# Kernel tuning notes

Measured on AMD Instinct MI355X. Metric: run time of the kernel, lower is better.

## Reference

```python
import jax, jax.numpy as jnp
import numpy as np

C = 256
G = 16
EPS = 1e-5


def conv1x1(x, w):
    # x: [N,C,H,W], w: [Cout,Cin]
    return jnp.einsum('nchw,oc->nohw', x, w)


def group_norm(x, gamma, beta, groups=G, eps=EPS):
    n, c, h, w = x.shape
    xg = x.reshape(n, groups, c // groups, h, w)
    mu = xg.mean(axis=(2, 3, 4), keepdims=True)
    var = ((xg - mu) ** 2).mean(axis=(2, 3, 4), keepdims=True)
    xn = ((xg - mu) * jax.lax.rsqrt(var + eps)).reshape(n, c, h, w)
    return xn * gamma[:, None, None] + beta[:, None, None]


def silu(x):
    return x * jax.nn.sigmoid(x)


def scan(x, axis, reverse=False):
    if reverse:
        return jnp.flip(jnp.cumsum(jnp.flip(x, axis), axis=axis), axis)
    return jnp.cumsum(x, axis=axis)


def depthwise3x3(x, w_dw):
    # w_dw: [C,1,3,3], groups=C
    return jax.lax.conv_general_dilated(
        x, w_dw, window_strides=(1, 1), padding=((1, 1), (1, 1)),
        dimension_numbers=('NCHW', 'OIHW', 'NCHW'), feature_group_count=x.shape[1])


def setup_inputs() -> dict:
    key = jax.random.key(0)
    ks = jax.random.split(key, 5)
    N, H, W = 8, 80, 80
    s1 = 1.0 / np.sqrt(C)
    return {
        'x': jax.random.normal(ks[0], (N, C, H, W), jnp.float32),
        'w_pre': jax.random.normal(ks[1], (C, C), jnp.float32) * s1,
        'g1': jnp.ones((C,), jnp.float32),
        'b1': jnp.zeros((C,), jnp.float32),
        'w_gate': jax.random.normal(ks[2], (C, C), jnp.float32) * s1,
        'b_gate': jnp.zeros((C,), jnp.float32),
        'w_dw': jax.random.normal(ks[3], (C, 1, 3, 3), jnp.float32) * (1.0 / 3.0),
        'w_pw': jax.random.normal(ks[4], (C, C), jnp.float32) * s1,
        'g2': jnp.ones((C,), jnp.float32),
        'b2': jnp.zeros((C,), jnp.float32),
    }


def reference(x, w_pre, g1, b1, w_gate, b_gate, w_dw, w_pw, g2, b2):
    # pre: 1x1 conv -> GroupNorm -> SiLU
    h = silu(group_norm(conv1x1(x, w_pre), g1, b1))
    # 4-directional cumulative scans
    lr = scan(h, 3, False)
    rl = scan(h, 3, True)
    tb = scan(h, 2, False)
    bt = scan(h, 2, True)
    fused = (lr + rl + tb + bt) * 0.25
    # sigmoid gate from pre features
    gate = jax.nn.sigmoid(conv1x1(h, w_gate) + b_gate[:, None, None])
    gated = fused * gate
    # mix: depthwise 3x3 -> 1x1 -> GroupNorm -> SiLU
    y = depthwise3x3(gated, w_dw)
    y = conv1x1(y, w_pw)
    return silu(group_norm(y, g2, b2))
```

## Files before the change

### kernel.cpp

```cpp
#include <hip/hip_runtime.h>
#include <stdint.h>

#define CC 256
#define HH 80
#define WW 80
#define PP 6400
#define GG 16
#define GNCNT (16*6400)
#define SAPAD 272

using frag_ab = __attribute__((ext_vector_type(8))) short;
using frag_cd = __attribute__((ext_vector_type(4))) float;
typedef unsigned short u16;

__device__ __forceinline__ float b2f(u16 u) {
    union { float f; uint32_t i; } v; v.i = ((uint32_t)u) << 16; return v.f;
}
__device__ __forceinline__ u16 f2b(float f) {
    uint32_t x = __float_as_uint(f);
    return (u16)((x + 0x7fffu + ((x >> 16) & 1u)) >> 16);
}
__device__ __forceinline__ float sigf(float x) { return 1.f / (1.f + __expf(-x)); }

__global__ __launch_bounds__(256) void cvt_kernel(const float* __restrict__ src,
                                                  u16* __restrict__ dst, int n4) {
    int i = blockIdx.x * 256 + threadIdx.x;
    if (i < n4) {
        float4 v = ((const float4*)src)[i];
        ushort4 o;
        o.x = f2b(v.x); o.y = f2b(v.y); o.z = f2b(v.z); o.w = f2b(v.w);
        ((ushort4*)dst)[i] = o;
    }
}

template<int MODE>
__global__ __launch_bounds__(256, 3) void gemm_kernel(
    const u16* __restrict__ A,
    const u16* __restrict__ Wb,
    u16* __restrict__ Out,
    float* __restrict__ pstats,
    const float* __restrict__ Srow,
    const float* __restrict__ Scol,
    const float* __restrict__ bgate,
    const float* __restrict__ Xf)
{
    __shared__ __align__(16) u16 sA[64 * SAPAD];

    const int t    = threadIdx.x;
    const int lane = t & 63;
    const int wave = t >> 6;
    const int m    = lane & 15;
    const int q    = lane >> 4;
    const int mt   = blockIdx.x;
    const int m0   = mt * 64;
    const int n    = mt / 100;
    const int o0w  = wave * 64;

    if (MODE == 0) {
        const int cl = t >> 2, pq = t & 3;
        const int p0 = m0 - n * PP;
        #pragma unroll
        for (int cb = 0; cb < 4; cb++) {
            const int c = cb * 64 + cl;
            const float* row = Xf + ((size_t)(n * CC + c)) * PP + p0 + pq * 16;
            #pragma unroll
            for (int u = 0; u < 4; u++) {
                float4 v = ((const float4*)(row + u * 4))[0];
                const int pp = pq * 16 + u * 4;
                sA[(pp + 0) * SAPAD + c] = f2b(v.x);
                sA[(pp + 1) * SAPAD + c] = f2b(v.y);
                sA[(pp + 2) * SAPAD + c] = f2b(v.z);
                sA[(pp + 3) * SAPAD + c] = f2b(v.w);
            }
        }
    } else {
        const int row = t >> 2, qt = t & 3;
        const u16* g = A + (size_t)(m0 + row) * CC + qt * 64;
        u16* d = sA + row * SAPAD + qt * 64;
        #pragma unroll
        for (int i = 0; i < 8; i++)
            *(frag_ab*)(d + i * 8) = *(const frag_ab*)(g + i * 8);
    }
    __syncthreads();

    frag_cd acc[4][4];
    #pragma unroll
    for (int ms = 0; ms < 4; ms++)
        #pragma unroll
        for (int j = 0; j < 4; j++)
            #pragma unroll
            for (int k = 0; k < 4; k++) acc[ms][j][k] = 0.f;

    const u16* wl = Wb + (size_t)(o0w + m) * CC + q * 8;

    #pragma unroll
    for (int jh = 0; jh < 2; jh++) {
        frag_ab wf[2][8];
        #pragma unroll
        for (int jj = 0; jj < 2; jj++)
            #pragma unroll
            for (int kc = 0; kc < 8; kc++)
                wf[jj][kc] = *(const frag_ab*)(wl + (size_t)((jh * 2 + jj) * 16) * CC + kc * 32);
        #pragma unroll
        for (int jj = 0; jj < 2; jj++)
            #pragma unroll
            for (int kc = 0; kc < 8; kc++)
                asm volatile("" : "+v"(wf[jj][kc]));

        #pragma unroll
        for (int ms = 0; ms < 4; ms++) {
            #pragma unroll
            for (int kc = 0; kc < 8; kc++) {
                frag_ab af = *(const frag_ab*)(sA + (ms * 16 + m) * SAPAD + kc * 32 + q * 8);
                #pragma unroll
                for (int jj = 0; jj < 2; jj++)
                    acc[ms][jh * 2 + jj] = __builtin_amdgcn_mfma_f32_16x16x32_bf16(
                        af, wf[jj][kc], acc[ms][jh * 2 + jj], 0, 0, 0);
            }
        }
    }

    ushort4 hv[4][4];
    if (MODE == 1) {
        const int rr0 = lane >> 4;
        const int cH  = o0w + (lane & 15) * 4;
        #pragma unroll
        for (int ms = 0; ms < 4; ms++)
            #pragma unroll
            for (int u = 0; u < 4; u++)
                hv[ms][u] = *(const ushort4*)(sA + (size_t)(ms * 16 + u * 4 + rr0) * SAPAD + cH);
    }
    __syncthreads();

    if (MODE == 0 || MODE == 2) {
        #pragma unroll
        for (int j = 0; j < 4; j++) {
            float s = 0.f, sq = 0.f;
            #pragma unroll
            for (int ms = 0; ms < 4; ms++)
                #pragma unroll
                for (int r = 0; r < 4; r++) {
                    float v = acc[ms][j][r];
                    s += v; sq += v * v;
                }
            #pragma unroll
            for (int off = 32; off > 0; off >>= 1) {
                s  += __shfl_down(s, off);
                sq += __shfl_down(sq, off);
            }
            if (lane == 0) {
                float* p = pstats + (size_t)mt * 32;
                p[wave * 4 + j]      = s;
                p[16 + wave * 4 + j] = sq;
            }
        }
        u16* myT = sA + wave * 1152;
        #pragma unroll
        for (int ms = 0; ms < 4; ms++) {
            #pragma unroll
            for (int j = 0; j < 4; j++)
                #pragma unroll
                for (int r = 0; r < 4; r++)
                    myT[(q * 4 + r) * 72 + j * 16 + m] = f2b(acc[ms][j][r]);
            #pragma unroll
            for (int u = 0; u < 2; u++) {
                const int rr = u * 8 + (lane >> 3);
                frag_ab v = *(const frag_ab*)(myT + rr * 72 + (lane & 7) * 8);
                *(frag_ab*)(Out + (size_t)(m0 + ms * 16 + rr) * CC + o0w + (lane & 7) * 8) = v;
            }
        }
    } else {
        float* myG = (float*)sA + wave * 1152;
        float bg[4];
        #pragma unroll
        for (int j = 0; j < 4; j++) bg[j] = bgate[o0w + j * 16 + m];
        #pragma unroll
        for (int ms = 0; ms < 4; ms++) {
            #pragma unroll
            for (int j = 0; j < 4; j++)
                #pragma unroll
                for (int r = 0; r < 4; r++)
                    myG[(q * 4 + r) * 72 + j * 16 + m] = sigf(acc[ms][j][r] + bg[j]);
            #pragma unroll
            for (int u = 0; u < 4; u++) {
                const int rr  = u * 4 + (lane >> 4);
                const int col = (lane & 15) * 4;
                float4 g4 = *(const float4*)(myG + rr * 72 + col);
                const int row = m0 + ms * 16 + rr;
                const int pl  = row - n * PP;
                const int pr  = pl / WW;
                const int pc  = pl - pr * WW;
                const int o   = o0w + col;
                ushort4 hq = hv[ms][u];
                float4  sr = *(const float4*)(Srow + (size_t)(n * HH + pr) * CC + o);
                float4  sc = *(const float4*)(Scol + (size_t)(n * HH + pc) * CC + o);
                ushort4 ov;
                ov.x = f2b(0.25f * (sr.x + sc.x + 2.f * b2f(hq.x)) * g4.x);
                ov.y = f2b(0.25f * (sr.y + sc.y + 2.f * b2f(hq.y)) * g4.y);
                ov.z = f2b(0.25f * (sr.z + sc.z + 2.f * b2f(hq.z)) * g4.z);
                ov.w = f2b(0.25f * (sr.w + sc.w + 2.f * b2f(hq.w)) * g4.w);
                *(ushort4*)(Out + (size_t)row * CC + o) = ov;
            }
        }
    }
}

__global__ __launch_bounds__(256) void gn1_kernel(
    const u16* __restrict__ c1, u16* __restrict__ hb,
    float* __restrict__ Srow,
    const float* __restrict__ pscr,
    const float* __restrict__ g1, const float* __restrict__ b1)
{
    __shared__ float sred[8 * 256];
    __shared__ float sstat[32];
    const int i = blockIdx.x, n = blockIdx.y;
    const int t = threadIdx.x;
    if (t < 32) {
        const int kind = t >> 4, g = t & 15;
        const float* p = pscr + (size_t)(n * 100) * 32 + kind * 16 + g;
        float s = 0.f;
        #pragma unroll 4
        for (int ii = 0; ii < 100; ii++) s += p[ii * 32];
        sstat[t] = s;
    }
    __syncthreads();

    const int jg = t >> 5, cc = t & 31;
    const int c8 = cc * 8;
    const int g  = cc >> 1;
    const float su   = sstat[g];
    const float sq   = sstat[16 + g];
    const float mean = su * (1.f / GNCNT);
    const float var  = sq * (1.f / GNCNT) - mean * mean;
    const float inv  = rsqrtf(var + 1e-5f);
    float a[8], b[8];
    #pragma unroll
    for (int k = 0; k < 8; k++) {
        a[k] = inv * g1[c8 + k];
        b[k] = b1[c8 + k] - mean * a[k];
    }
    float srow8[8];
    #pragma unroll
    for (int k = 0; k < 8; k++) srow8[k] = 0.f;

    const size_t base = (size_t)(n * PP + i * WW) * CC;
    for (int s = 0; s < 10; s++) {
        const int j = jg + s * 8;
        const u16* src = c1 + base + (size_t)j * CC + c8;
        u16*       dst = hb + base + (size_t)j * CC + c8;
        frag_ab v = *(const frag_ab*)src;
        frag_ab o;
        #pragma unroll
        for (int k = 0; k < 8; k++) {
            float xn = b2f((u16)v[k]) * a[k] + b[k];
            float hs = xn * sigf(xn);
            o[k] = (short)f2b(hs);
            srow8[k] += hs;
        }
        *(frag_ab*)dst = o;
    }
    #pragma unroll
    for (int k = 0; k < 8; k++) sred[jg * 256 + c8 + k] = srow8[k];
    __syncthreads();
    {
        const int c = t;
        float s = 0.f;
        #pragma unroll
        for (int k = 0; k < 8; k++) s += sred[k * 256 + c];
        Srow[(size_t)(n * HH + i) * CC + c] = s;
    }
}

__global__ __launch_bounds__(256) void scol_kernel(
    const u16* __restrict__ hb, float* __restrict__ Scol)
{
    const int jg = blockIdx.x, iq = blockIdx.y, n = blockIdx.z;
    const int t = threadIdx.x;
    const int js = t >> 5, cc = t & 31;
    const int j = jg * 8 + js, c8 = cc * 8;
    float acc8[8];
    #pragma unroll
    for (int k = 0; k < 8; k++) acc8[k] = 0.f;
    for (int s = 0; s < 20; s++) {
        const int i = iq * 20 + s;
        frag_ab v = *(const frag_ab*)(hb + (size_t)(n * PP + i * WW + j) * CC + c8);
        #pragma unroll
        for (int k = 0; k < 8; k++) acc8[k] += b2f((u16)v[k]);
    }
    float* dst = Scol + (size_t)(n * HH + j) * CC + c8;
    #pragma unroll
    for (int k = 0; k < 8; k++) atomicAdd(&dst[k], acc8[k]);
}

__global__ __launch_bounds__(256) void dw_kernel(
    const u16* __restrict__ gin, u16* __restrict__ dout,
    const float* __restrict__ wdw)
{
    __shared__ float sw[1152];
    const int i = blockIdx.x, chalf = blockIdx.y, n = blockIdx.z;
    const int t = threadIdx.x;
    for (int u = t; u < 1152; u += 256) sw[u] = wdw[chalf * 1152 + u];
    __syncthreads();

    const int jg = t >> 5, cc = t & 31;
    const int gc = chalf * 128 + cc * 4;
    float wl[4][9];
    #pragma unroll
    for (int cl = 0; cl < 4; cl++)
        #pragma unroll
        for (int k = 0; k < 9; k++) wl[cl][k] = sw[(cc * 4 + cl) * 9 + k];

    const size_t nbase = (size_t)n * PP * CC;
    for (int s = 0; s < 10; s++) {
        const int j = jg + s * 8;
        float acc4[4] = {0.f, 0.f, 0.f, 0.f};
        #pragma unroll
        for (int di = -1; di <= 1; di++) {
            const int ii = i + di;
            if (ii < 0 || ii >= HH) continue;
            #pragma unroll
            for (int dj = -1; dj <= 1; dj++) {
                const int jj = j + dj;
                if (jj < 0 || jj >= WW) continue;
                ushort4 v = *(const ushort4*)(gin + nbase + (size_t)(ii * WW + jj) * CC + gc);
                const int k = (di + 1) * 3 + (dj + 1);
                acc4[0] += wl[0][k] * b2f(v.x);
                acc4[1] += wl[1][k] * b2f(v.y);
                acc4[2] += wl[2][k] * b2f(v.z);
                acc4[3] += wl[3][k] * b2f(v.w);
            }
        }
        ushort4 o;
        o.x = f2b(acc4[0]); o.y = f2b(acc4[1]); o.z = f2b(acc4[2]); o.w = f2b(acc4[3]);
        *(ushort4*)(dout + nbase + (size_t)(i * WW + j) * CC + gc) = o;
    }
}

__global__ __launch_bounds__(256) void gn2T_kernel(
    const u16* __restrict__ Y, float* __restrict__ out,
    const float* __restrict__ pscr,
    const float* __restrict__ g2, const float* __restrict__ b2v)
{
    __shared__ u16 sT[64 * 72];
    __shared__ float sstat[32];
    const int p0 = blockIdx.x * 64, c0 = blockIdx.y * 64, n = blockIdx.z;
    const int t = threadIdx.x;
    if (t < 32) {
        const int kind = t >> 4, g = t & 15;
        const float* p = pscr + (size_t)(n * 100) * 32 + kind * 16 + g;
        float s = 0.f;
        #pragma unroll 4
        for (int ii = 0; ii < 100; ii++) s += p[ii * 32];
        sstat[t] = s;
    }
    {
        const int pl = t >> 2, cq = t & 3;
        const u16* row = Y + (size_t)(n * PP + p0 + pl) * CC + c0 + cq * 16;
        *(frag_ab*)(sT + pl * 72 + cq * 16)     = *(const frag_ab*)(row);
        *(frag_ab*)(sT + pl * 72 + cq * 16 + 8) = *(const frag_ab*)(row + 8);
    }
    __syncthreads();
    {
        const int cl = t >> 2, pq = t & 3;
        const int c = c0 + cl, g = c >> 4;
        const float su   = sstat[g];
        const float sq   = sstat[16 + g];
        const float mean = su * (1.f / GNCNT);
        const float var  = sq * (1.f / GNCNT) - mean * mean;
        const float inv  = rsqrtf(var + 1e-5f);
        const float a    = inv * g2[c];
        const float b    = b2v[c] - mean * a;
        float* orow = out + (size_t)(n * CC + c) * PP + p0 + pq * 16;
        #pragma unroll
        for (int u4 = 0; u4 < 4; u4++) {
            float4 o;
            float* op = (float*)&o;
            #pragma unroll
            for (int e = 0; e < 4; e++) {
                const int pp = pq * 16 + u4 * 4 + e;
                float xn = b2f(sT[pp * 72 + cl]) * a + b;
                op[e] = xn * sigf(xn);
            }
            ((float4*)(orow + u4 * 4))[0] = o;
        }
    }
}

extern "C" void kernel_launch(void* const* d_in, const int* in_sizes, int n_in,
                              void* d_out, int out_size, void* d_ws, size_t ws_size,
                              hipStream_t stream)
{
    const float* x      = (const float*)d_in[0];
    const float* w_pre  = (const float*)d_in[1];
    const float* g1     = (const float*)d_in[2];
    const float* b1     = (const float*)d_in[3];
    const float* w_gate = (const float*)d_in[4];
    const float* b_gate = (const float*)d_in[5];
    const float* w_dw   = (const float*)d_in[6];
    const float* w_pw   = (const float*)d_in[7];
    const float* g2     = (const float*)d_in[8];
    const float* b2     = (const float*)d_in[9];
    float* out = (float*)d_out;

    char* ws = (char*)d_ws;
    u16*   wb0   = (u16*)(ws);
    u16*   wb1   = (u16*)(ws + 131072);
    u16*   wb2   = (u16*)(ws + 262144);
    u16*   bufA  = (u16*)(ws + 26607616);
    u16*   bufB  = (u16*)(ws + 52822016);
    float* Srow  = (float*)(ws + 79036416);
    float* Scol  = (float*)(ws + 79691776);
    float* pscr0 = (float*)(ws + 80347136);
    float* pscr1 = (float*)(ws + 80449536);

    hipMemsetAsync(Scol, 0, 655360, stream);

    cvt_kernel<<<64, 256, 0, stream>>>(w_pre,  wb0, 16384);
    cvt_kernel<<<64, 256, 0, stream>>>(w_gate, wb1, 16384);
    cvt_kernel<<<64, 256, 0, stream>>>(w_pw,   wb2, 16384);

    gemm_kernel<0><<<800, 256, 0, stream>>>(nullptr, wb0, bufA, pscr0,
                                            nullptr, nullptr, nullptr, x);
    gn1_kernel<<<dim3(80, 8), 256, 0, stream>>>(bufA, bufB, Srow, pscr0, g1, b1);
    scol_kernel<<<dim3(10, 4, 8), 256, 0, stream>>>(bufB, Scol);
    gemm_kernel<1><<<800, 256, 0, stream>>>(bufB, wb1, bufA, nullptr,
                                            Srow, Scol, b_gate, nullptr);
    dw_kernel<<<dim3(80, 2, 8), 256, 0, stream>>>(bufA, bufB, w_dw);
    gemm_kernel<2><<<800, 256, 0, stream>>>(bufB, wb2, bufA, pscr1,
                                            nullptr, nullptr, nullptr, nullptr);
    gn2T_kernel<<<dim3(100, 4, 8), 256, 0, stream>>>(bufA, out, pscr1, g2, b2);
}
```

Baseline: 305.6 us.

## Process two tiles per GEMM block with register prefetch; drop atomics and memset

GEMM modes 1 and 2 now launch 400 blocks, and each block handles two 64-row tiles. The second tile's A data is prefetched into registers while the first tile computes, then written to LDS. The scol kernel writes per-quarter partial column sums instead of using atomicAdd, which removes the memset; the gate GEMM epilogue sums the four partials. The three weight conversions are merged into one launch, and some barriers become explicit waitcnt+s_barrier. The cost is more register pressure (launch bounds occupancy drops to 2 for these modes) and four times more Scol reads in the epilogue.

Measured after the change: 324.4 us. 6.1% more time.

```diff
diff --git a/kernel.cpp b/kernel.cpp
--- a/kernel.cpp
+++ b/kernel.cpp
@@ -22,66 +22,38 @@
 }
 __device__ __forceinline__ float sigf(float x) { return 1.f / (1.f + __expf(-x)); }
 
-__global__ __launch_bounds__(256) void cvt_kernel(const float* __restrict__ src,
-                                                  u16* __restrict__ dst, int n4) {
-    int i = blockIdx.x * 256 + threadIdx.x;
-    if (i < n4) {
-        float4 v = ((const float4*)src)[i];
-        ushort4 o;
-        o.x = f2b(v.x); o.y = f2b(v.y); o.z = f2b(v.z); o.w = f2b(v.w);
-        ((ushort4*)dst)[i] = o;
-    }
-}
+__device__ __forceinline__ void bar_lgkm() {
+    asm volatile("s_waitcnt lgkmcnt(0)\n\ts_barrier" ::: "memory");
+}
+
+__global__ __launch_bounds__(256) void cvt3_kernel(
+    const float* __restrict__ s0, const float* __restrict__ s1,
+    const float* __restrict__ s2,
+    u16* __restrict__ d0, u16* __restrict__ d1, u16* __restrict__ d2)
+{
+    const int blk = blockIdx.x >> 6;
+    const int i = (blockIdx.x & 63) * 256 + threadIdx.x;
+    const float* s = (blk == 0) ? s0 : (blk == 1) ? s1 : s2;
+    u16*         d = (blk == 0) ? d0 : (blk == 1) ? d1 : d2;
+    float4 v = ((const float4*)s)[i];
+    ushort4 o;
+    o.x = f2b(v.x); o.y = f2b(v.y); o.z = f2b(v.z); o.w = f2b(v.w);
+    ((ushort4*)d)[i] = o;
+}
+
 
 template<int MODE>
-__global__ __launch_bounds__(256, 3) void gemm_kernel(
-    const u16* __restrict__ A,
+__device__ __forceinline__ void tile_body(
+    u16* sA, int mt,
     const u16* __restrict__ Wb,
-    u16* __restrict__ Out,
-    float* __restrict__ pstats,
-    const float* __restrict__ Srow,
-    const float* __restrict__ Scol,
+    u16* __restrict__ Out, float* __restrict__ pstats,
+    const float* __restrict__ Srow, const float* __restrict__ Scolp,
     const float* __restrict__ bgate,
-    const float* __restrict__ Xf)
-{
-    __shared__ __align__(16) u16 sA[64 * SAPAD];
-
-    const int t    = threadIdx.x;
-    const int lane = t & 63;
-    const int wave = t >> 6;
-    const int m    = lane & 15;
-    const int q    = lane >> 4;
-    const int mt   = blockIdx.x;
-    const int m0   = mt * 64;
-    const int n    = mt / 100;
-    const int o0w  = wave * 64;
-
-    if (MODE == 0) {
-        const int cl = t >> 2, pq = t & 3;
-        const int p0 = m0 - n * PP;
-        #pragma unroll
-        for (int cb = 0; cb < 4; cb++) {
-            const int c = cb * 64 + cl;
-            const float* row = Xf + ((size_t)(n * CC + c)) * PP + p0 + pq * 16;
-            #pragma unroll
-            for (int u = 0; u < 4; u++) {
-                float4 v = ((const float4*)(row + u * 4))[0];
-                const int pp = pq * 16 + u * 4;
-                sA[(pp + 0) * SAPAD + c] = f2b(v.x);
-                sA[(pp + 1) * SAPAD + c] = f2b(v.y);
-                sA[(pp + 2) * SAPAD + c] = f2b(v.z);
-                sA[(pp + 3) * SAPAD + c] = f2b(v.w);
-            }
-        }
-    } else {
-        const int row = t >> 2, qt = t & 3;
-        const u16* g = A + (size_t)(m0 + row) * CC + qt * 64;
-        u16* d = sA + row * SAPAD + qt * 64;
-        #pragma unroll
-        for (int i = 0; i < 8; i++)
-            *(frag_ab*)(d + i * 8) = *(const frag_ab*)(g + i * 8);
-    }
-    __syncthreads();
+    int lane, int wave, int m, int q)
+{
+    const int m0  = mt * 64;
+    const int n   = mt / 100;
+    const int o0w = wave * 64;
 
     frag_cd acc[4][4];
     #pragma unroll
@@ -130,7 +102,7 @@
             for (int u = 0; u < 4; u++)
                 hv[ms][u] = *(const ushort4*)(sA + (size_t)(ms * 16 + u * 4 + rr0) * SAPAD + cH);
     }
-    __syncthreads();
+    bar_lgkm();
 
     if (MODE == 0 || MODE == 2) {
         #pragma unroll
@@ -193,7 +165,12 @@
                 const int o   = o0w + col;
                 ushort4 hq = hv[ms][u];
                 float4  sr = *(const float4*)(Srow + (size_t)(n * HH + pr) * CC + o);
-                float4  sc = *(const float4*)(Scol + (size_t)(n * HH + pc) * CC + o);
+                float4 sc; sc.x = sc.y = sc.z = sc.w = 0.f;
+                #pragma unroll
+                for (int iq = 0; iq < 4; iq++) {
+                    float4 v = *(const float4*)(Scolp + ((size_t)((iq * 8 + n) * HH + pc)) * CC + o);
+                    sc.x += v.x; sc.y += v.y; sc.z += v.z; sc.w += v.w;
+                }
                 ushort4 ov;
                 ov.x = f2b(0.25f * (sr.x + sc.x + 2.f * b2f(hq.x)) * g4.x);
                 ov.y = f2b(0.25f * (sr.y + sc.y + 2.f * b2f(hq.y)) * g4.y);
@@ -203,6 +180,87 @@
             }
         }
     }
+}
+
+template<int MODE>
+__global__ __launch_bounds__(256, (MODE == 0 ? 3 : 2)) void gemm_kernel(
+    const u16* __restrict__ A,
+    const u16* __restrict__ Wb,
+    u16* __restrict__ Out,
+    float* __restrict__ pstats,
+    const float* __restrict__ Srow,
+    const float* __restrict__ Scolp,
+    const float* __restrict__ bgate,
+    const float* __restrict__ Xf)
+{
+    __shared__ __align__(16) u16 sA[64 * SAPAD];
+
+    const int t    = threadIdx.x;
+    const int lane = t & 63;
+    const int wave = t >> 6;
+    const int m    = lane & 15;
+    const int q    = lane >> 4;
+
+    if (MODE == 0) {
+        const int mt = blockIdx.x;
+        const int n  = mt / 100;
+        const int cl = t >> 2, pq = t & 3;
+        const int p0 = mt * 64 - n * PP;
+        #pragma unroll
+        for (int cb = 0; cb < 4; cb++) {
+            const int c = cb * 64 + cl;
+            const float* row = Xf + ((size_t)(n * CC + c)) * PP + p0 + pq * 16;
+            #pragma unroll
+            for (int u = 0; u < 4; u++) {
+                float4 v = ((const float4*)(row + u * 4))[0];
+                const int pp = pq * 16 + u * 4;
+                sA[(pp + 0) * SAPAD + c] = f2b(v.x);
+                sA[(pp + 1) * SAPAD + c] = f2b(v.y);
+                sA[(pp + 2) * SAPAD + c] = f2b(v.z);
+                sA[(pp + 3) * SAPAD + c] = f2b(v.w);
+            }
+        }
+        __syncthreads();
+        tile_body<MODE>(sA, mt, Wb, Out, pstats, Srow, Scolp, bgate, lane, wave, m, q);
+        return;
+    }
+
+    const int mt0 = blockIdx.x;
+    const int mt1 = blockIdx.x + 400;
+    const int row = t >> 2, qt = t & 3;
+
+    {
+        const u16* g = A + (size_t)(mt0 * 64 + row) * CC + qt * 64;
+        u16* d = sA + row * SAPAD + qt * 64;
+        #pragma unroll
+        for (int i = 0; i < 8; i++)
+            *(frag_ab*)(d + i * 8) = *(const frag_ab*)(g + i * 8);
+    }
+    __syncthreads();
+
+    frag_ab P[8];
+    {
+        const u16* g = A + (size_t)(mt1 * 64 + row) * CC + qt * 64;
+        #pragma unroll
+        for (int i = 0; i < 8; i++)
+            P[i] = *(const frag_ab*)(g + i * 8);
+        #pragma unroll
+        for (int i = 0; i < 8; i++)
+            asm volatile("" : "+v"(P[i]));
+    }
+
+    tile_body<MODE>(sA, mt0, Wb, Out, pstats, Srow, Scolp, bgate, lane, wave, m, q);
+
+    bar_lgkm();
+    {
+        u16* d = sA + row * SAPAD + qt * 64;
+        #pragma unroll
+        for (int i = 0; i < 8; i++)
+            *(frag_ab*)(d + i * 8) = P[i];
+    }
+    bar_lgkm();
+
+    tile_body<MODE>(sA, mt1, Wb, Out, pstats, Srow, Scolp, bgate, lane, wave, m, q);
 }
 
 __global__ __launch_bounds__(256) void gn1_kernel(
@@ -272,7 +330,7 @@
 }
 
 __global__ __launch_bounds__(256) void scol_kernel(
-    const u16* __restrict__ hb, float* __restrict__ Scol)
+    const u16* __restrict__ hb, float* __restrict__ Scolp)
 {
     const int jg = blockIdx.x, iq = blockIdx.y, n = blockIdx.z;
     const int t = threadIdx.x;
@@ -287,9 +345,9 @@
         #pragma unroll
         for (int k = 0; k < 8; k++) acc8[k] += b2f((u16)v[k]);
     }
-    float* dst = Scol + (size_t)(n * HH + j) * CC + c8;
-    #pragma unroll
-    for (int k = 0; k < 8; k++) atomicAdd(&dst[k], acc8[k]);
+    float* dst = Scolp + ((size_t)((iq * 8 + n) * HH + j)) * CC + c8;
+    *(float4*)(dst)     = make_float4(acc8[0], acc8[1], acc8[2], acc8[3]);
+    *(float4*)(dst + 4) = make_float4(acc8[4], acc8[5], acc8[6], acc8[7]);
 }
 
 __global__ __launch_bounds__(256) void dw_kernel(
@@ -406,27 +464,23 @@
     u16*   wb0   = (u16*)(ws);
     u16*   wb1   = (u16*)(ws + 131072);
     u16*   wb2   = (u16*)(ws + 262144);
+    float* Scolp = (float*)(ws + 393216);
     u16*   bufA  = (u16*)(ws + 26607616);
     u16*   bufB  = (u16*)(ws + 52822016);
     float* Srow  = (float*)(ws + 79036416);
-    float* Scol  = (float*)(ws + 79691776);
     float* pscr0 = (float*)(ws + 80347136);
     float* pscr1 = (float*)(ws + 80449536);
 
-    hipMemsetAsync(Scol, 0, 655360, stream);
-
-    cvt_kernel<<<64, 256, 0, stream>>>(w_pre,  wb0, 16384);
-    cvt_kernel<<<64, 256, 0, stream>>>(w_gate, wb1, 16384);
-    cvt_kernel<<<64, 256, 0, stream>>>(w_pw,   wb2, 16384);
+    cvt3_kernel<<<192, 256, 0, stream>>>(w_pre, w_gate, w_pw, wb0, wb1, wb2);
 
     gemm_kernel<0><<<800, 256, 0, stream>>>(nullptr, wb0, bufA, pscr0,
                                             nullptr, nullptr, nullptr, x);
     gn1_kernel<<<dim3(80, 8), 256, 0, stream>>>(bufA, bufB, Srow, pscr0, g1, b1);
-    scol_kernel<<<dim3(10, 4, 8), 256, 0, stream>>>(bufB, Scol);
-    gemm_kernel<1><<<800, 256, 0, stream>>>(bufB, wb1, bufA, nullptr,
-                                            Srow, Scol, b_gate, nullptr);
+    scol_kernel<<<dim3(10, 4, 8), 256, 0, stream>>>(bufB, Scolp);
+    gemm_kernel<1><<<400, 256, 0, stream>>>(bufB, wb1, bufA, nullptr,
+                                            Srow, Scolp, b_gate, nullptr);
     dw_kernel<<<dim3(80, 2, 8), 256, 0, stream>>>(bufA, bufB, w_dw);
-    gemm_kernel<2><<<800, 256, 0, stream>>>(bufB, wb2, bufA, pscr1,
+    gemm_kernel<2><<<400, 256, 0, stream>>>(bufB, wb2, bufA, pscr1,
                                             nullptr, nullptr, nullptr, nullptr);
     gn2T_kernel<<<dim3(100, 4, 8), 256, 0, stream>>>(bufA, out, pscr1, g2, b2);
 }
```

## Fuse depthwise 3x3 conv into pointwise GEMM prologue and merge weight conversions

Applied to the files above, without the earlier changes.

The separate depthwise 3x3 kernel is removed. Each pointwise GEMM block now computes the depthwise conv for its 64 pixel rows straight into shared-memory A tiles, which avoids writing and re-reading the full intermediate bf16 tensor. The three weight-conversion launches are merged into one kernel. The cost is extra shared memory for the transposed weights, an extra barrier, and redundant halo loads inside the GEMM prologue, which may lower occupancy.

Result: slower. 352.9 us (+15.5%).

```diff
diff --git a/kernel.cpp b/kernel.cpp
--- a/kernel.cpp
+++ b/kernel.cpp
@@ -22,15 +22,19 @@
 }
 __device__ __forceinline__ float sigf(float x) { return 1.f / (1.f + __expf(-x)); }
 
-__global__ __launch_bounds__(256) void cvt_kernel(const float* __restrict__ src,
-                                                  u16* __restrict__ dst, int n4) {
-    int i = blockIdx.x * 256 + threadIdx.x;
-    if (i < n4) {
-        float4 v = ((const float4*)src)[i];
-        ushort4 o;
-        o.x = f2b(v.x); o.y = f2b(v.y); o.z = f2b(v.z); o.w = f2b(v.w);
-        ((ushort4*)dst)[i] = o;
-    }
+__global__ __launch_bounds__(256) void cvt3_kernel(
+    const float* __restrict__ s0, const float* __restrict__ s1,
+    const float* __restrict__ s2,
+    u16* __restrict__ d0, u16* __restrict__ d1, u16* __restrict__ d2)
+{
+    const int blk = blockIdx.x >> 6;
+    const int i = (blockIdx.x & 63) * 256 + threadIdx.x;
+    const float* s = (blk == 0) ? s0 : (blk == 1) ? s1 : s2;
+    u16*         d = (blk == 0) ? d0 : (blk == 1) ? d1 : d2;
+    float4 v = ((const float4*)s)[i];
+    ushort4 o;
+    o.x = f2b(v.x); o.y = f2b(v.y); o.z = f2b(v.z); o.w = f2b(v.w);
+    ((ushort4*)d)[i] = o;
 }
 
 template<int MODE>
@@ -42,9 +46,10 @@
     const float* __restrict__ Srow,
     const float* __restrict__ Scol,
     const float* __restrict__ bgate,
-    const float* __restrict__ Xf)
+    const float* __restrict__ Xfw)
 {
     __shared__ __align__(16) u16 sA[64 * SAPAD];
+    __shared__ float sw[(MODE == 2) ? 2304 : 1];
 
     const int t    = threadIdx.x;
     const int lane = t & 63;
@@ -62,7 +67,7 @@
         #pragma unroll
         for (int cb = 0; cb < 4; cb++) {
             const int c = cb * 64 + cl;
-            const float* row = Xf + ((size_t)(n * CC + c)) * PP + p0 + pq * 16;
+            const float* row = Xfw + ((size_t)(n * CC + c)) * PP + p0 + pq * 16;
             #pragma unroll
             for (int u = 0; u < 4; u++) {
                 float4 v = ((const float4*)(row + u * 4))[0];
@@ -72,6 +77,41 @@
                 sA[(pp + 2) * SAPAD + c] = f2b(v.z);
                 sA[(pp + 3) * SAPAD + c] = f2b(v.w);
             }
+        }
+    } else if (MODE == 2) {
+        for (int u = t; u < 2304; u += 256) {
+            const int c = u / 9, k = u - c * 9;
+            sw[k * 256 + c] = Xfw[u];
+        }
+        __syncthreads();
+        const int cc4 = (lane) * 4;
+        const int r0  = wave;
+        float4 wl[9];
+        #pragma unroll
+        for (int k = 0; k < 9; k++)
+            wl[k] = *(const float4*)(sw + k * 256 + cc4);
+        for (int s = 0; s < 16; s++) {
+            const int r  = r0 + s * 4;
+            const int p  = m0 + r - n * PP;
+            const int pr = p / WW, pc = p - pr * WW;
+            float a0 = 0.f, a1 = 0.f, a2 = 0.f, a3 = 0.f;
+            #pragma unroll
+            for (int di = -1; di <= 1; di++) {
+                const int ii = pr + di;
+                if (ii < 0 || ii >= HH) continue;
+                #pragma unroll
+                for (int dj = -1; dj <= 1; dj++) {
+                    const int jj = pc + dj;
+                    if (jj < 0 || jj >= WW) continue;
+                    ushort4 v = *(const ushort4*)(A + (size_t)(n * PP + ii * WW + jj) * CC + cc4);
+                    const float4 w = wl[(di + 1) * 3 + (dj + 1)];
+                    a0 += w.x * b2f(v.x); a1 += w.y * b2f(v.y);
+                    a2 += w.z * b2f(v.z); a3 += w.w * b2f(v.w);
+                }
+            }
+            ushort4 o;
+            o.x = f2b(a0); o.y = f2b(a1); o.z = f2b(a2); o.w = f2b(a3);
+            *(ushort4*)(sA + r * SAPAD + cc4) = o;
         }
     } else {
         const int row = t >> 2, qt = t & 3;
@@ -292,50 +332,6 @@
     for (int k = 0; k < 8; k++) atomicAdd(&dst[k], acc8[k]);
 }
 
-__global__ __launch_bounds__(256) void dw_kernel(
-    const u16* __restrict__ gin, u16* __restrict__ dout,
-    const float* __restrict__ wdw)
-{
-    __shared__ float sw[1152];
-    const int i = blockIdx.x, chalf = blockIdx.y, n = blockIdx.z;
-    const int t = threadIdx.x;
-    for (int u = t; u < 1152; u += 256) sw[u] = wdw[chalf * 1152 + u];
-    __syncthreads();
-
-    const int jg = t >> 5, cc = t & 31;
-    const int gc = chalf * 128 + cc * 4;
-    float wl[4][9];
-    #pragma unroll
-    for (int cl = 0; cl < 4; cl++)
-        #pragma unroll
-        for (int k = 0; k < 9; k++) wl[cl][k] = sw[(cc * 4 + cl) * 9 + k];
-
-    const size_t nbase = (size_t)n * PP * CC;
-    for (int s = 0; s < 10; s++) {
-        const int j = jg + s * 8;
-        float acc4[4] = {0.f, 0.f, 0.f, 0.f};
-        #pragma unroll
-        for (int di = -1; di <= 1; di++) {
-            const int ii = i + di;
-            if (ii < 0 || ii >= HH) continue;
-            #pragma unroll
-            for (int dj = -1; dj <= 1; dj++) {
-                const int jj = j + dj;
-                if (jj < 0 || jj >= WW) continue;
-                ushort4 v = *(const ushort4*)(gin + nbase + (size_t)(ii * WW + jj) * CC + gc);
-                const int k = (di + 1) * 3 + (dj + 1);
-                acc4[0] += wl[0][k] * b2f(v.x);
-                acc4[1] += wl[1][k] * b2f(v.y);
-                acc4[2] += wl[2][k] * b2f(v.z);
-                acc4[3] += wl[3][k] * b2f(v.w);
-            }
-        }
-        ushort4 o;
-        o.x = f2b(acc4[0]); o.y = f2b(acc4[1]); o.z = f2b(acc4[2]); o.w = f2b(acc4[3]);
-        *(ushort4*)(dout + nbase + (size_t)(i * WW + j) * CC + gc) = o;
-    }
-}
-
 __global__ __launch_bounds__(256) void gn2T_kernel(
     const u16* __restrict__ Y, float* __restrict__ out,
     const float* __restrict__ pscr,
@@ -415,9 +411,7 @@
 
     hipMemsetAsync(Scol, 0, 655360, stream);
 
-    cvt_kernel<<<64, 256, 0, stream>>>(w_pre,  wb0, 16384);
-    cvt_kernel<<<64, 256, 0, stream>>>(w_gate, wb1, 16384);
-    cvt_kernel<<<64, 256, 0, stream>>>(w_pw,   wb2, 16384);
+    cvt3_kernel<<<192, 256, 0, stream>>>(w_pre, w_gate, w_pw, wb0, wb1, wb2);
 
     gemm_kernel<0><<<800, 256, 0, stream>>>(nullptr, wb0, bufA, pscr0,
                                             nullptr, nullptr, nullptr, x);
@@ -425,8 +419,7 @@
     scol_kernel<<<dim3(10, 4, 8), 256, 0, stream>>>(bufB, Scol);
     gemm_kernel<1><<<800, 256, 0, stream>>>(bufB, wb1, bufA, nullptr,
                                             Srow, Scol, b_gate, nullptr);
-    dw_kernel<<<dim3(80, 2, 8), 256, 0, stream>>>(bufA, bufB, w_dw);
-    gemm_kernel<2><<<800, 256, 0, stream>>>(bufB, wb2, bufA, pscr1,
-                                            nullptr, nullptr, nullptr, nullptr);
-    gn2T_kernel<<<dim3(100, 4, 8), 256, 0, stream>>>(bufA, out, pscr1, g2, b2);
-}
+    gemm_kernel<2><<<800, 256, 0, stream>>>(bufA, wb2, bufB, pscr1,
+                                            nullptr, nullptr, nullptr, w_dw);
+    gn2T_kernel<<<dim3(100, 4, 8), 256, 0, stream>>>(bufB, out, pscr1, g2, b2);
+}
```

## Recompute GroupNorm1+SiLU in consumers instead of materializing activations

Applied to the files above, without the earlier changes.

The normalized and activated tensor h is no longer written to global memory. The row-sum, column-sum and gate-GEMM kernels each read the raw conv output and recompute GroupNorm and SiLU from the partial statistics; the gate GEMM does this while staging its A tile into shared memory. The aim is to remove one full bf16 activation write and the pass that produced it. In exchange each consumer recomputes the sigmoid, and the group statistics are reduced redundantly in every block. The three weight-conversion launches are also merged into one kernel.

After: 318.1 us. 1.04x slower.

```diff
diff --git a/kernel.cpp b/kernel.cpp
--- a/kernel.cpp
+++ b/kernel.cpp
@@ -22,15 +22,19 @@
 }
 __device__ __forceinline__ float sigf(float x) { return 1.f / (1.f + __expf(-x)); }
 
-__global__ __launch_bounds__(256) void cvt_kernel(const float* __restrict__ src,
-                                                  u16* __restrict__ dst, int n4) {
-    int i = blockIdx.x * 256 + threadIdx.x;
-    if (i < n4) {
-        float4 v = ((const float4*)src)[i];
-        ushort4 o;
-        o.x = f2b(v.x); o.y = f2b(v.y); o.z = f2b(v.z); o.w = f2b(v.w);
-        ((ushort4*)dst)[i] = o;
-    }
+__global__ __launch_bounds__(256) void cvt3_kernel(
+    const float* __restrict__ s0, const float* __restrict__ s1,
+    const float* __restrict__ s2,
+    u16* __restrict__ d0, u16* __restrict__ d1, u16* __restrict__ d2)
+{
+    const int blk = blockIdx.x >> 6;
+    const int i = (blockIdx.x & 63) * 256 + threadIdx.x;
+    const float* s = (blk == 0) ? s0 : (blk == 1) ? s1 : s2;
+    u16*         d = (blk == 0) ? d0 : (blk == 1) ? d1 : d2;
+    float4 v = ((const float4*)s)[i];
+    ushort4 o;
+    o.x = f2b(v.x); o.y = f2b(v.y); o.z = f2b(v.z); o.w = f2b(v.w);
+    ((ushort4*)d)[i] = o;
 }
 
 template<int MODE>
@@ -42,9 +46,13 @@
     const float* __restrict__ Srow,
     const float* __restrict__ Scol,
     const float* __restrict__ bgate,
-    const float* __restrict__ Xf)
+    const float* __restrict__ Xf,
+    const float* __restrict__ g1v,
+    const float* __restrict__ b1v)
 {
     __shared__ __align__(16) u16 sA[64 * SAPAD];
+    __shared__ float sstat[32];
+    __shared__ float sAB[512];
 
     const int t    = threadIdx.x;
     const int lane = t & 63;
@@ -72,6 +80,41 @@
                 sA[(pp + 2) * SAPAD + c] = f2b(v.z);
                 sA[(pp + 3) * SAPAD + c] = f2b(v.w);
             }
+        }
+    } else if (MODE == 1) {
+        if (t < 32) {
+            const int kind = t >> 4, g = t & 15;
+            const float* p = pstats + (size_t)(n * 100) * 32 + kind * 16 + g;
+            float s = 0.f;
+            #pragma unroll 4
+            for (int ii = 0; ii < 100; ii++) s += p[ii * 32];
+            sstat[t] = s;
+        }
+        __syncthreads();
+        {
+            const int c = t, g = c >> 4;
+            const float mean = sstat[g] * (1.f / GNCNT);
+            const float var  = sstat[16 + g] * (1.f / GNCNT) - mean * mean;
+            const float inv  = rsqrtf(var + 1e-5f);
+            const float a    = inv * g1v[c];
+            sAB[c]       = a;
+            sAB[256 + c] = b1v[c] - mean * a;
+        }
+        __syncthreads();
+        const int row = t >> 2, qt = t & 3;
+        const u16* g = A + (size_t)(m0 + row) * CC + qt * 64;
+        u16* d = sA + row * SAPAD + qt * 64;
+        #pragma unroll
+        for (int i = 0; i < 8; i++) {
+            frag_ab v = *(const frag_ab*)(g + i * 8);
+            const int cb = qt * 64 + i * 8;
+            frag_ab o;
+            #pragma unroll
+            for (int e = 0; e < 8; e++) {
+                float xn = b2f((u16)v[e]) * sAB[cb + e] + sAB[256 + cb + e];
+                o[e] = (short)f2b(xn * sigf(xn));
+            }
+            *(frag_ab*)(d + i * 8) = o;
         }
     } else {
         const int row = t >> 2, qt = t & 3;
@@ -205,8 +248,8 @@
     }
 }
 
-__global__ __launch_bounds__(256) void gn1_kernel(
-    const u16* __restrict__ c1, u16* __restrict__ hb,
+__global__ __launch_bounds__(256) void srow_kernel(
+    const u16* __restrict__ c1,
     float* __restrict__ Srow,
     const float* __restrict__ pscr,
     const float* __restrict__ g1, const float* __restrict__ b1)
@@ -246,18 +289,12 @@
     const size_t base = (size_t)(n * PP + i * WW) * CC;
     for (int s = 0; s < 10; s++) {
         const int j = jg + s * 8;
-        const u16* src = c1 + base + (size_t)j * CC + c8;
-        u16*       dst = hb + base + (size_t)j * CC + c8;
-        frag_ab v = *(const frag_ab*)src;
-        frag_ab o;
+        frag_ab v = *(const frag_ab*)(c1 + base + (size_t)j * CC + c8);
         #pragma unroll
         for (int k = 0; k < 8; k++) {
             float xn = b2f((u16)v[k]) * a[k] + b[k];
-            float hs = xn * sigf(xn);
-            o[k] = (short)f2b(hs);
-            srow8[k] += hs;
-        }
-        *(frag_ab*)dst = o;
+            srow8[k] += xn * sigf(xn);
+        }
     }
     #pragma unroll
     for (int k = 0; k < 8; k++) sred[jg * 256 + c8 + k] = srow8[k];
@@ -272,20 +309,46 @@
 }
 
 __global__ __launch_bounds__(256) void scol_kernel(
-    const u16* __restrict__ hb, float* __restrict__ Scol)
-{
+    const u16* __restrict__ c1, float* __restrict__ Scol,
+    const float* __restrict__ pscr,
+    const float* __restrict__ g1, const float* __restrict__ b1)
+{
+    __shared__ float sstat[32];
     const int jg = blockIdx.x, iq = blockIdx.y, n = blockIdx.z;
     const int t = threadIdx.x;
+    if (t < 32) {
+        const int kind = t >> 4, g = t & 15;
+        const float* p = pscr + (size_t)(n * 100) * 32 + kind * 16 + g;
+        float s = 0.f;
+        #pragma unroll 4
+        for (int ii = 0; ii < 100; ii++) s += p[ii * 32];
+        sstat[t] = s;
+    }
+    __syncthreads();
+
     const int js = t >> 5, cc = t & 31;
     const int j = jg * 8 + js, c8 = cc * 8;
+    const int g = cc >> 1;
+    const float mean = sstat[g] * (1.f / GNCNT);
+    const float var  = sstat[16 + g] * (1.f / GNCNT) - mean * mean;
+    const float inv  = rsqrtf(var + 1e-5f);
+    float a[8], b[8];
+    #pragma unroll
+    for (int k = 0; k < 8; k++) {
+        a[k] = inv * g1[c8 + k];
+        b[k] = b1[c8 + k] - mean * a[k];
+    }
     float acc8[8];
     #pragma unroll
     for (int k = 0; k < 8; k++) acc8[k] = 0.f;
     for (int s = 0; s < 20; s++) {
         const int i = iq * 20 + s;
-        frag_ab v = *(const frag_ab*)(hb + (size_t)(n * PP + i * WW + j) * CC + c8);
-        #pragma unroll
-        for (int k = 0; k < 8; k++) acc8[k] += b2f((u16)v[k]);
+        frag_ab v = *(const frag_ab*)(c1 + (size_t)(n * PP + i * WW + j) * CC + c8);
+        #pragma unroll
+        for (int k = 0; k < 8; k++) {
+            float xn = b2f((u16)v[k]) * a[k] + b[k];
+            acc8[k] += xn * sigf(xn);
+        }
     }
     float* dst = Scol + (size_t)(n * HH + j) * CC + c8;
     #pragma unroll
@@ -415,18 +478,18 @@
 
     hipMemsetAsync(Scol, 0, 655360, stream);
 
-    cvt_kernel<<<64, 256, 0, stream>>>(w_pre,  wb0, 16384);
-    cvt_kernel<<<64, 256, 0, stream>>>(w_gate, wb1, 16384);
-    cvt_kernel<<<64, 256, 0, stream>>>(w_pw,   wb2, 16384);
+    cvt3_kernel<<<192, 256, 0, stream>>>(w_pre, w_gate, w_pw, wb0, wb1, wb2);
 
     gemm_kernel<0><<<800, 256, 0, stream>>>(nullptr, wb0, bufA, pscr0,
-                                            nullptr, nullptr, nullptr, x);
-    gn1_kernel<<<dim3(80, 8), 256, 0, stream>>>(bufA, bufB, Srow, pscr0, g1, b1);
-    scol_kernel<<<dim3(10, 4, 8), 256, 0, stream>>>(bufB, Scol);
-    gemm_kernel<1><<<800, 256, 0, stream>>>(bufB, wb1, bufA, nullptr,
-                                            Srow, Scol, b_gate, nullptr);
-    dw_kernel<<<dim3(80, 2, 8), 256, 0, stream>>>(bufA, bufB, w_dw);
-    gemm_kernel<2><<<800, 256, 0, stream>>>(bufB, wb2, bufA, pscr1,
-                                            nullptr, nullptr, nullptr, nullptr);
-    gn2T_kernel<<<dim3(100, 4, 8), 256, 0, stream>>>(bufA, out, pscr1, g2, b2);
-}
+                                            nullptr, nullptr, nullptr, x,
+                                            nullptr, nullptr);
+    srow_kernel<<<dim3(80, 8), 256, 0, stream>>>(bufA, Srow, pscr0, g1, b1);
+    scol_kernel<<<dim3(10, 4, 8), 256, 0, stream>>>(bufA, Scol, pscr0, g1, b1);
+    gemm_kernel<1><<<800, 256, 0, stream>>>(bufA, wb1, bufB, pscr0,
+                                            Srow, Scol, b_gate, nullptr, g1, b1);
+    dw_kernel<<<dim3(80, 2, 8), 256, 0, stream>>>(bufB, bufA, w_dw);
+    gemm_kernel<2><<<800, 256, 0, stream>>>(bufA, wb2, bufB, pscr1,
+                                            nullptr, nullptr, nullptr, nullptr,
+                                            nullptr, nullptr);
+    gn2T_kernel<<<dim3(100, 4, 8), 256, 0, stream>>>(bufB, out, pscr1, g2, b2);
+}
```
